# Performance work log

Hardware: AMD Instinct MI355X
Metric: run time of the kernel (lower is better)

The kernel has to match this reference:

```python
import jax, jax.numpy as jnp
import numpy as np

N = 4096          # number of leaves
M = 2 * N - 1     # total tree nodes
B = 256           # batch of distribution pairs


def setup_inputs() -> dict:
    key = jax.random.key(0)
    k0, k1, k2, k3, k4, k5 = jax.random.split(key, 6)
    # ancestor-indicator matrix: mostly zeros (structured sparse used densely)
    subtree = (jax.random.uniform(k0, (M, N)) < 0.01).astype(jnp.float32)
    d1 = jax.random.uniform(k1, (N, B), dtype=jnp.float32)
    d2 = jax.random.uniform(k2, (N, B), dtype=jnp.float32)
    ot_distances = jax.random.uniform(k3, (B,), dtype=jnp.float32)
    param = jax.random.normal(k4, (M,), dtype=jnp.float32)
    parents = jax.random.randint(k5, (M,), 0, M, dtype=jnp.int32)
    return {"d1": d1, "d2": d2, "ot_distances": ot_distances,
            "subtree": subtree, "param": param, "parents": parents}


def reference(d1, d2, ot_distances, subtree, param, parents):
    # aggregate leaf mass to every tree node: [M, B]
    m_d1 = jnp.matmul(subtree, d1)
    m_d2 = jnp.matmul(subtree, d2)
    # edge weight = parent height - node height: [M]
    w_v = param[parents] - param
    # tree-Wasserstein-1 per pair: [B]
    w1_tree = 0.5 * jnp.matmul(w_v, jnp.abs(m_d1 - m_d2))
    return jnp.sum(jnp.square(ot_distances - w1_tree))
```

## Files before the change

### kernel.cpp

```cpp
#include <hip/hip_runtime.h>
#include <hip/hip_fp8.h>

#define NN    4096
#define MM    8191
#define BB    256
#define CAP   256

typedef float nfloat4 __attribute__((ext_vector_type(4)));
typedef float f32x2 __attribute__((ext_vector_type(2)));

__device__ __forceinline__ int prefix_lt(unsigned long long m) {
    return __builtin_amdgcn_mbcnt_hi((unsigned)(m >> 32),
           __builtin_amdgcn_mbcnt_lo((unsigned)m, 0u));
}

#if defined(__has_builtin)
#if __has_builtin(__builtin_amdgcn_cvt_pk_fp8_f32) && __has_builtin(__builtin_amdgcn_cvt_pk_f32_fp8)
#define HW_FP8 1
#endif
#endif

__device__ __forceinline__ unsigned pack4fp8(float x0, float x1, float x2, float x3) {
#ifdef HW_FP8
    int r = 0;
    r = __builtin_amdgcn_cvt_pk_fp8_f32(x0, x1, r, false);
    r = __builtin_amdgcn_cvt_pk_fp8_f32(x2, x3, r, true);
    return (unsigned)r;
#else
    __hip_fp8_e4m3 a(x0), b(x1), c(x2), d(x3);
    return (unsigned)a.__x | ((unsigned)b.__x << 8) |
           ((unsigned)c.__x << 16) | ((unsigned)d.__x << 24);
#endif
}

__global__ __launch_bounds__(256) void k_prep(const float4* __restrict__ d1,
                                              const float4* __restrict__ d2,
                                              float* __restrict__ part2,
                                              unsigned* __restrict__ dd8) {
    int idx = blockIdx.x * 256 + threadIdx.x;
    if (idx < 256 * BB) part2[idx] = 0.0f;
    float4 a = d1[idx], b = d2[idx];
    dd8[idx] = pack4fp8(a.x - b.x, a.y - b.y, a.z - b.z, a.w - b.w);
}

__global__ __launch_bounds__(256, 4) void k_fused(
        const nfloat4* __restrict__ st4,
        const unsigned* __restrict__ dd8,
        const float* __restrict__ param,
        const int*   __restrict__ parents,
        float* __restrict__ part2) {
    __shared__ unsigned short s_idx[4][CAP];
    __shared__ float s_part[BB];
    const int tid  = threadIdx.x;
    const int wave = tid >> 6;
    const int lane = tid & 63;
    unsigned short* buf = s_idx[wave];

    s_part[tid] = 0.0f;
    __syncthreads();

    const int m = blockIdx.x * 4 + wave;
    if (m < MM) {
        int c = 0;
        #pragma unroll
        for (int h = 0; h < 2; ++h) {
            const nfloat4* base = st4 + (size_t)m * (NN / 4) + h * (NN / 8);
            nfloat4 v0 = __builtin_nontemporal_load(base + lane);
            nfloat4 v1 = __builtin_nontemporal_load(base + 64  + lane);
            nfloat4 v2 = __builtin_nontemporal_load(base + 128 + lane);
            nfloat4 v3 = __builtin_nontemporal_load(base + 192 + lane);
            nfloat4 v4 = __builtin_nontemporal_load(base + 256 + lane);
            nfloat4 v5 = __builtin_nontemporal_load(base + 320 + lane);
            nfloat4 v6 = __builtin_nontemporal_load(base + 384 + lane);
            nfloat4 v7 = __builtin_nontemporal_load(base + 448 + lane);

            const int cb = h * (NN / 2);
            #define SITE(val, col)                                          \
            {                                                               \
                unsigned long long mk = __ballot((val) != 0.0f);            \
                if ((val) != 0.0f)                                          \
                    buf[c + prefix_lt(mk)] = (unsigned short)(col);         \
                c += __popcll(mk);                                          \
            }
            #define QUAD(v, cb0)                                            \
                SITE(v.x, (cb0))     SITE(v.y, (cb0) + 1)                   \
                SITE(v.z, (cb0) + 2) SITE(v.w, (cb0) + 3)
            QUAD(v0, cb + (lane)       * 4)
            QUAD(v1, cb + (64  + lane) * 4)
            QUAD(v2, cb + (128 + lane) * 4)
            QUAD(v3, cb + (192 + lane) * 4)
            QUAD(v4, cb + (256 + lane) * 4)
            QUAD(v5, cb + (320 + lane) * 4)
            QUAD(v6, cb + (384 + lane) * 4)
            QUAD(v7, cb + (448 + lane) * 4)
            #undef QUAD
            #undef SITE
        }
        __builtin_amdgcn_wave_barrier();

        float c0 = 0.f, c1 = 0.f, c2 = 0.f, c3 = 0.f;
        float e0 = 0.f, e1 = 0.f, e2 = 0.f, e3 = 0.f;
#ifdef HW_FP8
        #define DEC(u, j0, j1, j2, j3)                                       \
        {                                                                    \
            f32x2 lo = __builtin_amdgcn_cvt_pk_f32_fp8((int)(u), false);     \
            f32x2 hi = __builtin_amdgcn_cvt_pk_f32_fp8((int)(u), true);      \
            j0 += lo.x; j1 += lo.y; j2 += hi.x; j3 += hi.y;                  \
        }
#else
        #define DEC(u, j0, j1, j2, j3)                                       \
        {                                                                    \
            __hip_fp8_e4m3 q0, q1, q2, q3;                                   \
            q0.__x = (unsigned char)(u);                                     \
            q1.__x = (unsigned char)((u) >> 8);                              \
            q2.__x = (unsigned char)((u) >> 16);                             \
            q3.__x = (unsigned char)((u) >> 24);                             \
            j0 += (float)q0; j1 += (float)q1; j2 += (float)q2; j3 += (float)q3; \
        }
#endif
        #define ACCA(u) DEC(u, c0, c1, c2, c3)
        #define ACCB(u) DEC(u, e0, e1, e2, e3)
        const unsigned* lw = (const unsigned*)buf;
        int i = 0;
        for (; i + 8 <= c; i += 8) {
            unsigned q0 = lw[(i >> 1)    ];
            unsigned q1 = lw[(i >> 1) + 1];
            unsigned q2 = lw[(i >> 1) + 2];
            unsigned q3 = lw[(i >> 1) + 3];
            unsigned g0 = dd8[(q0 & 0xffffu) * 64u + lane];
            unsigned g1 = dd8[(q0 >> 16)     * 64u + lane];
            unsigned g2 = dd8[(q1 & 0xffffu) * 64u + lane];
            unsigned g3 = dd8[(q1 >> 16)     * 64u + lane];
            unsigned g4 = dd8[(q2 & 0xffffu) * 64u + lane];
            unsigned g5 = dd8[(q2 >> 16)     * 64u + lane];
            unsigned g6 = dd8[(q3 & 0xffffu) * 64u + lane];
            unsigned g7 = dd8[(q3 >> 16)     * 64u + lane];
            ACCA(g0) ACCB(g1) ACCA(g2) ACCB(g3)
            ACCA(g4) ACCB(g5) ACCA(g6) ACCB(g7)
        }
        for (; i + 4 <= c; i += 4) {
            unsigned q0 = lw[(i >> 1)    ];
            unsigned q1 = lw[(i >> 1) + 1];
            unsigned g0 = dd8[(q0 & 0xffffu) * 64u + lane];
            unsigned g1 = dd8[(q0 >> 16)     * 64u + lane];
            unsigned g2 = dd8[(q1 & 0xffffu) * 64u + lane];
            unsigned g3 = dd8[(q1 >> 16)     * 64u + lane];
            ACCA(g0) ACCB(g1) ACCA(g2) ACCB(g3)
        }
        for (; i < c; ++i) {
            unsigned g = dd8[(unsigned)buf[i] * 64u + lane];
            ACCA(g)
        }
        #undef ACCA
        #undef ACCB
        #undef DEC

        const float wgt = param[parents[m]] - param[m];
        atomicAdd(&s_part[4 * lane + 0], wgt * fabsf(c0 + e0));
        atomicAdd(&s_part[4 * lane + 1], wgt * fabsf(c1 + e1));
        atomicAdd(&s_part[4 * lane + 2], wgt * fabsf(c2 + e2));
        atomicAdd(&s_part[4 * lane + 3], wgt * fabsf(c3 + e3));
    }
    __syncthreads();
    atomicAdd(&part2[(size_t)(blockIdx.x & 255) * BB + tid], s_part[tid]);
}

__global__ __launch_bounds__(1024) void k_finalize(const float* __restrict__ part2,
                                                   const float* __restrict__ ot,
                                                   float* __restrict__ out) {
    __shared__ float s_red[4][BB];
    __shared__ float s_sq[16];
    const int tid = threadIdx.x;
    const int s = tid >> 8, b = tid & 255;

    float a0 = 0.f, a1 = 0.f, a2 = 0.f, a3 = 0.f;
    float a4 = 0.f, a5 = 0.f, a6 = 0.f, a7 = 0.f;
    #pragma unroll
    for (int j = 0; j < 64; j += 8) {
        int row = s * 64 + j;
        a0 += part2[(row    ) * BB + b];
        a1 += part2[(row + 1) * BB + b];
        a2 += part2[(row + 2) * BB + b];
        a3 += part2[(row + 3) * BB + b];
        a4 += part2[(row + 4) * BB + b];
        a5 += part2[(row + 5) * BB + b];
        a6 += part2[(row + 6) * BB + b];
        a7 += part2[(row + 7) * BB + b];
    }
    s_red[s][b] = ((a0 + a1) + (a2 + a3)) + ((a4 + a5) + (a6 + a7));
    __syncthreads();

    float v = 0.0f;
    if (s == 0) {
        float w1 = (s_red[0][b] + s_red[1][b]) + (s_red[2][b] + s_red[3][b]);
        float e = ot[b] - 0.5f * w1;
        v = e * e;
    }
    #pragma unroll
    for (int off = 32; off > 0; off >>= 1) v += __shfl_down(v, off, 64);
    if ((tid & 63) == 0) s_sq[tid >> 6] = v;
    __syncthreads();
    if (tid == 0) out[0] = (s_sq[0] + s_sq[1]) + (s_sq[2] + s_sq[3]);
}

extern "C" void kernel_launch(void* const* d_in, const int* in_sizes, int n_in,
                              void* d_out, int out_size, void* d_ws, size_t ws_size,
                              hipStream_t stream) {
    const float* d1      = (const float*)d_in[0];
    const float* d2      = (const float*)d_in[1];
    const float* ot      = (const float*)d_in[2];
    const float* subtree = (const float*)d_in[3];
    const float* param   = (const float*)d_in[4];
    const int*   parents = (const int*)d_in[5];

    char* wsb = (char*)d_ws;
    float* part2   = (float*)wsb;
    unsigned* dd8  = (unsigned*)(wsb + 256 * BB * 4);

    k_prep<<<1024, 256, 0, stream>>>((const float4*)d1, (const float4*)d2,
                                     part2, dd8);
    k_fused<<<2048, 256, 0, stream>>>((const nfloat4*)subtree, dd8,
                                      param, parents, part2);
    k_finalize<<<1, 1024, 0, stream>>>(part2, ot, (float*)d_out);
}
```

Before: 47.25 us.

## Replicate packed fp8 difference table per XCD to localize gathers

The prep kernel now writes eight copies of the fp8-packed d1-d2 table when the workspace is large enough. Each block of the fused kernel reads the copy selected by its block index modulo eight, matching round-robin placement of blocks across dies. The aim is to keep each die's random gathers in its own L2 rather than sharing lines across dies. In exchange, the prep kernel does eight times the writes and re-reads of the inputs, and uses more workspace.

```diff
diff --git a/kernel.cpp b/kernel.cpp
--- a/kernel.cpp
+++ b/kernel.cpp
@@ -36,11 +36,16 @@
 __global__ __launch_bounds__(256) void k_prep(const float4* __restrict__ d1,
                                               const float4* __restrict__ d2,
                                               float* __restrict__ part2,
-                                              unsigned* __restrict__ dd8) {
-    int idx = blockIdx.x * 256 + threadIdx.x;
-    if (idx < 256 * BB) part2[idx] = 0.0f;
+                                              unsigned* __restrict__ dd8,
+                                              int repmask) {
+    const int p   = blockIdx.x;
+    const int r   = p & repmask;
+    const int s   = p >> (repmask ? 3 : 0);
+    const int idx = s * 256 + (int)threadIdx.x;
+    if (r == 0 && idx < 256 * BB) part2[idx] = 0.0f;
     float4 a = d1[idx], b = d2[idx];
-    dd8[idx] = pack4fp8(a.x - b.x, a.y - b.y, a.z - b.z, a.w - b.w);
+    dd8[(size_t)r * (NN * BB / 4) + idx] =
+        pack4fp8(a.x - b.x, a.y - b.y, a.z - b.z, a.w - b.w);
 }
 
 __global__ __launch_bounds__(256, 4) void k_fused(
@@ -48,13 +53,15 @@
         const unsigned* __restrict__ dd8,
         const float* __restrict__ param,
         const int*   __restrict__ parents,
-        float* __restrict__ part2) {
+        float* __restrict__ part2,
+        int repmask) {
     __shared__ unsigned short s_idx[4][CAP];
     __shared__ float s_part[BB];
     const int tid  = threadIdx.x;
     const int wave = tid >> 6;
     const int lane = tid & 63;
     unsigned short* buf = s_idx[wave];
+    const unsigned* ddl = dd8 + (size_t)(blockIdx.x & repmask) * (NN * BB / 4);
 
     s_part[tid] = 0.0f;
     __syncthreads();
@@ -127,28 +134,28 @@
             unsigned q1 = lw[(i >> 1) + 1];
             unsigned q2 = lw[(i >> 1) + 2];
             unsigned q3 = lw[(i >> 1) + 3];
-            unsigned g0 = dd8[(q0 & 0xffffu) * 64u + lane];
-            unsigned g1 = dd8[(q0 >> 16)     * 64u + lane];
-            unsigned g2 = dd8[(q1 & 0xffffu) * 64u + lane];
-            unsigned g3 = dd8[(q1 >> 16)     * 64u + lane];
-            unsigned g4 = dd8[(q2 & 0xffffu) * 64u + lane];
-            unsigned g5 = dd8[(q2 >> 16)     * 64u + lane];
-            unsigned g6 = dd8[(q3 & 0xffffu) * 64u + lane];
-            unsigned g7 = dd8[(q3 >> 16)     * 64u + lane];
+            unsigned g0 = ddl[(q0 & 0xffffu) * 64u + lane];
+            unsigned g1 = ddl[(q0 >> 16)     * 64u + lane];
+            unsigned g2 = ddl[(q1 & 0xffffu) * 64u + lane];
+            unsigned g3 = ddl[(q1 >> 16)     * 64u + lane];
+            unsigned g4 = ddl[(q2 & 0xffffu) * 64u + lane];
+            unsigned g5 = ddl[(q2 >> 16)     * 64u + lane];
+            unsigned g6 = ddl[(q3 & 0xffffu) * 64u + lane];
+            unsigned g7 = ddl[(q3 >> 16)     * 64u + lane];
             ACCA(g0) ACCB(g1) ACCA(g2) ACCB(g3)
             ACCA(g4) ACCB(g5) ACCA(g6) ACCB(g7)
         }
         for (; i + 4 <= c; i += 4) {
             unsigned q0 = lw[(i >> 1)    ];
             unsigned q1 = lw[(i >> 1) + 1];
-            unsigned g0 = dd8[(q0 & 0xffffu) * 64u + lane];
-            unsigned g1 = dd8[(q0 >> 16)     * 64u + lane];
-            unsigned g2 = dd8[(q1 & 0xffffu) * 64u + lane];
-            unsigned g3 = dd8[(q1 >> 16)     * 64u + lane];
+            unsigned g0 = ddl[(q0 & 0xffffu) * 64u + lane];
+            unsigned g1 = ddl[(q0 >> 16)     * 64u + lane];
+            unsigned g2 = ddl[(q1 & 0xffffu) * 64u + lane];
+            unsigned g3 = ddl[(q1 >> 16)     * 64u + lane];
             ACCA(g0) ACCB(g1) ACCA(g2) ACCB(g3)
         }
         for (; i < c; ++i) {
-            unsigned g = dd8[(unsigned)buf[i] * 64u + lane];
+            unsigned g = ddl[(unsigned)buf[i] * 64u + lane];
             ACCA(g)
         }
         #undef ACCA
@@ -214,12 +221,16 @@
     const int*   parents = (const int*)d_in[5];
 
     char* wsb = (char*)d_ws;
-    float* part2   = (float*)wsb;
-    unsigned* dd8  = (unsigned*)(wsb + 256 * BB * 4);
-
-    k_prep<<<1024, 256, 0, stream>>>((const float4*)d1, (const float4*)d2,
-                                     part2, dd8);
+    float* part2  = (float*)wsb;
+    unsigned* dd8 = (unsigned*)(wsb + 256 * BB * 4);
+
+    const size_t need8 = 256 * BB * 4 + (size_t)8 * NN * BB;
+    const int nrep = (ws_size >= need8) ? 8 : 1;
+    const int repmask = nrep - 1;
+
+    k_prep<<<1024 * nrep, 256, 0, stream>>>((const float4*)d1, (const float4*)d2,
+                                            part2, dd8, repmask);
     k_fused<<<2048, 256, 0, stream>>>((const nfloat4*)subtree, dd8,
-                                      param, parents, part2);
+                                      param, parents, part2, repmask);
     k_finalize<<<1, 1024, 0, stream>>>(part2, ot, (float*)d_out);
 }
```

Result: slower. 56.47 us (+19.5%).

## Split compaction from gather and stage batch slabs of dd8 in shared memory

Applied to the files above, without the earlier changes.

The fused kernel is split in two. A compaction kernel writes per-row nonzero column lists to global memory. A slab kernel then loads a 16-column batch slab of the FP8 difference matrix (64 KB) into LDS and gathers from LDS instead of from global/L2. Blocks are tiled over 16 batch slabs and 32 row groups, and partial sums are written directly instead of with global atomics. The cost is an extra launch, a global round trip for the index lists, and 64 KB of LDS per block, which limits occupancy.

```diff
diff --git a/kernel.cpp b/kernel.cpp
--- a/kernel.cpp
+++ b/kernel.cpp
@@ -5,6 +5,9 @@
 #define MM    8191
 #define BB    256
 #define CAP   256
+#define NSLAB 16
+#define SLABW 16
+#define NPART 512
 
 typedef float nfloat4 __attribute__((ext_vector_type(4)));
 typedef float f32x2 __attribute__((ext_vector_type(2)));
@@ -33,136 +36,155 @@
 #endif
 }
 
+__device__ __forceinline__ void dec4fp8(unsigned g, float& x0, float& x1,
+                                        float& x2, float& x3) {
+#ifdef HW_FP8
+    f32x2 lo = __builtin_amdgcn_cvt_pk_f32_fp8((int)g, false);
+    f32x2 hi = __builtin_amdgcn_cvt_pk_f32_fp8((int)g, true);
+    x0 = lo.x; x1 = lo.y; x2 = hi.x; x3 = hi.y;
+#else
+    __hip_fp8_e4m3 q0, q1, q2, q3;
+    q0.__x = (unsigned char)g;
+    q1.__x = (unsigned char)(g >> 8);
+    q2.__x = (unsigned char)(g >> 16);
+    q3.__x = (unsigned char)(g >> 24);
+    x0 = (float)q0; x1 = (float)q1; x2 = (float)q2; x3 = (float)q3;
+#endif
+}
+
 __global__ __launch_bounds__(256) void k_prep(const float4* __restrict__ d1,
                                               const float4* __restrict__ d2,
                                               float* __restrict__ part2,
                                               unsigned* __restrict__ dd8) {
     int idx = blockIdx.x * 256 + threadIdx.x;
-    if (idx < 256 * BB) part2[idx] = 0.0f;
+    if (idx < NPART * BB) part2[idx] = 0.0f;
     float4 a = d1[idx], b = d2[idx];
     dd8[idx] = pack4fp8(a.x - b.x, a.y - b.y, a.z - b.z, a.w - b.w);
 }
 
-__global__ __launch_bounds__(256, 4) void k_fused(
+__global__ __launch_bounds__(256, 4) void k_compact(
         const nfloat4* __restrict__ st4,
+        int* __restrict__ cnt,
+        unsigned short* __restrict__ list) {
+    __shared__ unsigned short s_buf[4][CAP];
+    const int wave = threadIdx.x >> 6;
+    const int lane = threadIdx.x & 63;
+    unsigned short* buf = s_buf[wave];
+    const int m = blockIdx.x * 4 + wave;
+    if (m >= MM) return;
+
+    int c = 0;
+    #pragma unroll
+    for (int h = 0; h < 2; ++h) {
+        const nfloat4* base = st4 + (size_t)m * (NN / 4) + h * (NN / 8);
+        nfloat4 v0 = __builtin_nontemporal_load(base + lane);
+        nfloat4 v1 = __builtin_nontemporal_load(base + 64  + lane);
+        nfloat4 v2 = __builtin_nontemporal_load(base + 128 + lane);
+        nfloat4 v3 = __builtin_nontemporal_load(base + 192 + lane);
+        nfloat4 v4 = __builtin_nontemporal_load(base + 256 + lane);
+        nfloat4 v5 = __builtin_nontemporal_load(base + 320 + lane);
+        nfloat4 v6 = __builtin_nontemporal_load(base + 384 + lane);
+        nfloat4 v7 = __builtin_nontemporal_load(base + 448 + lane);
+
+        const int cb = h * (NN / 2);
+        #define SITE(val, col)                                          \
+        {                                                               \
+            unsigned long long mk = __ballot((val) != 0.0f);            \
+            if ((val) != 0.0f)                                          \
+                buf[c + prefix_lt(mk)] = (unsigned short)(col);         \
+            c += __popcll(mk);                                          \
+        }
+        #define QUAD(v, cb0)                                            \
+            SITE(v.x, (cb0))     SITE(v.y, (cb0) + 1)                   \
+            SITE(v.z, (cb0) + 2) SITE(v.w, (cb0) + 3)
+        QUAD(v0, cb + (lane)       * 4)
+        QUAD(v1, cb + (64  + lane) * 4)
+        QUAD(v2, cb + (128 + lane) * 4)
+        QUAD(v3, cb + (192 + lane) * 4)
+        QUAD(v4, cb + (256 + lane) * 4)
+        QUAD(v5, cb + (320 + lane) * 4)
+        QUAD(v6, cb + (384 + lane) * 4)
+        QUAD(v7, cb + (448 + lane) * 4)
+        #undef QUAD
+        #undef SITE
+    }
+    __builtin_amdgcn_wave_barrier();
+
+    if (lane == 0) cnt[m] = c;
+    uint4* lv = (uint4*)(list + (size_t)m * CAP);
+    const int nv = (c + 7) >> 3;
+    if (lane < nv) lv[lane] = ((const uint4*)s_buf[wave])[lane];
+}
+
+__global__ __launch_bounds__(512, 4) void k_slab(
         const unsigned* __restrict__ dd8,
+        const int* __restrict__ cnt,
+        const unsigned short* __restrict__ list,
         const float* __restrict__ param,
         const int*   __restrict__ parents,
         float* __restrict__ part2) {
-    __shared__ unsigned short s_idx[4][CAP];
-    __shared__ float s_part[BB];
+    __shared__ unsigned s_dd[NN * 4];
+    __shared__ float s_part[SLABW];
     const int tid  = threadIdx.x;
     const int wave = tid >> 6;
     const int lane = tid & 63;
-    unsigned short* buf = s_idx[wave];
-
-    s_part[tid] = 0.0f;
-    __syncthreads();
-
-    const int m = blockIdx.x * 4 + wave;
-    if (m < MM) {
-        int c = 0;
+    const int s    = blockIdx.x & (NSLAB - 1);
+    const int rg   = blockIdx.x >> 4;
+
+    if (tid < SLABW) s_part[tid] = 0.0f;
+    #pragma unroll
+    for (int i = 0; i < 32; ++i) {
+        int t = tid + i * 512;
+        int n = t >> 2, j = t & 3;
+        s_dd[t] = dd8[(size_t)n * 64 + s * 4 + j];
+    }
+    __syncthreads();
+
+    const int j   = lane & 3;
+    const int sub = lane >> 2;
+    float p0 = 0.f, p1 = 0.f, p2 = 0.f, p3 = 0.f;
+
+    for (int r = 0; r < 32; ++r) {
+        const int m = rg * 256 + wave * 32 + r;
+        if (m >= MM) break;
+        int c = cnt[m];
+        if (c > CAP) c = CAP;
+        const unsigned short* lp = list + (size_t)m * CAP;
+
+        float a0 = 0.f, a1 = 0.f, a2 = 0.f, a3 = 0.f;
+        for (int it = 0; it * 16 < c; ++it) {
+            int i = it * 16 + sub;
+            if (i < c) {
+                unsigned n = lp[i];
+                unsigned g = s_dd[n * 4 + j];
+                float x0, x1, x2, x3;
+                dec4fp8(g, x0, x1, x2, x3);
+                a0 += x0; a1 += x1; a2 += x2; a3 += x3;
+            }
+        }
         #pragma unroll
-        for (int h = 0; h < 2; ++h) {
-            const nfloat4* base = st4 + (size_t)m * (NN / 4) + h * (NN / 8);
-            nfloat4 v0 = __builtin_nontemporal_load(base + lane);
-            nfloat4 v1 = __builtin_nontemporal_load(base + 64  + lane);
-            nfloat4 v2 = __builtin_nontemporal_load(base + 128 + lane);
-            nfloat4 v3 = __builtin_nontemporal_load(base + 192 + lane);
-            nfloat4 v4 = __builtin_nontemporal_load(base + 256 + lane);
-            nfloat4 v5 = __builtin_nontemporal_load(base + 320 + lane);
-            nfloat4 v6 = __builtin_nontemporal_load(base + 384 + lane);
-            nfloat4 v7 = __builtin_nontemporal_load(base + 448 + lane);
-
-            const int cb = h * (NN / 2);
-            #define SITE(val, col)                                          \
-            {                                                               \
-                unsigned long long mk = __ballot((val) != 0.0f);            \
-                if ((val) != 0.0f)                                          \
-                    buf[c + prefix_lt(mk)] = (unsigned short)(col);         \
-                c += __popcll(mk);                                          \
-            }
-            #define QUAD(v, cb0)                                            \
-                SITE(v.x, (cb0))     SITE(v.y, (cb0) + 1)                   \
-                SITE(v.z, (cb0) + 2) SITE(v.w, (cb0) + 3)
-            QUAD(v0, cb + (lane)       * 4)
-            QUAD(v1, cb + (64  + lane) * 4)
-            QUAD(v2, cb + (128 + lane) * 4)
-            QUAD(v3, cb + (192 + lane) * 4)
-            QUAD(v4, cb + (256 + lane) * 4)
-            QUAD(v5, cb + (320 + lane) * 4)
-            QUAD(v6, cb + (384 + lane) * 4)
-            QUAD(v7, cb + (448 + lane) * 4)
-            #undef QUAD
-            #undef SITE
+        for (int off = 4; off <= 32; off <<= 1) {
+            a0 += __shfl_xor(a0, off, 64);
+            a1 += __shfl_xor(a1, off, 64);
+            a2 += __shfl_xor(a2, off, 64);
+            a3 += __shfl_xor(a3, off, 64);
         }
-        __builtin_amdgcn_wave_barrier();
-
-        float c0 = 0.f, c1 = 0.f, c2 = 0.f, c3 = 0.f;
-        float e0 = 0.f, e1 = 0.f, e2 = 0.f, e3 = 0.f;
-#ifdef HW_FP8
-        #define DEC(u, j0, j1, j2, j3)                                       \
-        {                                                                    \
-            f32x2 lo = __builtin_amdgcn_cvt_pk_f32_fp8((int)(u), false);     \
-            f32x2 hi = __builtin_amdgcn_cvt_pk_f32_fp8((int)(u), true);      \
-            j0 += lo.x; j1 += lo.y; j2 += hi.x; j3 += hi.y;                  \
-        }
-#else
-        #define DEC(u, j0, j1, j2, j3)                                       \
-        {                                                                    \
-            __hip_fp8_e4m3 q0, q1, q2, q3;                                   \
-            q0.__x = (unsigned char)(u);                                     \
-            q1.__x = (unsigned char)((u) >> 8);                              \
-            q2.__x = (unsigned char)((u) >> 16);                             \
-            q3.__x = (unsigned char)((u) >> 24);                             \
-            j0 += (float)q0; j1 += (float)q1; j2 += (float)q2; j3 += (float)q3; \
-        }
-#endif
-        #define ACCA(u) DEC(u, c0, c1, c2, c3)
-        #define ACCB(u) DEC(u, e0, e1, e2, e3)
-        const unsigned* lw = (const unsigned*)buf;
-        int i = 0;
-        for (; i + 8 <= c; i += 8) {
-            unsigned q0 = lw[(i >> 1)    ];
-            unsigned q1 = lw[(i >> 1) + 1];
-            unsigned q2 = lw[(i >> 1) + 2];
-            unsigned q3 = lw[(i >> 1) + 3];
-            unsigned g0 = dd8[(q0 & 0xffffu) * 64u + lane];
-            unsigned g1 = dd8[(q0 >> 16)     * 64u + lane];
-            unsigned g2 = dd8[(q1 & 0xffffu) * 64u + lane];
-            unsigned g3 = dd8[(q1 >> 16)     * 64u + lane];
-            unsigned g4 = dd8[(q2 & 0xffffu) * 64u + lane];
-            unsigned g5 = dd8[(q2 >> 16)     * 64u + lane];
-            unsigned g6 = dd8[(q3 & 0xffffu) * 64u + lane];
-            unsigned g7 = dd8[(q3 >> 16)     * 64u + lane];
-            ACCA(g0) ACCB(g1) ACCA(g2) ACCB(g3)
-            ACCA(g4) ACCB(g5) ACCA(g6) ACCB(g7)
-        }
-        for (; i + 4 <= c; i += 4) {
-            unsigned q0 = lw[(i >> 1)    ];
-            unsigned q1 = lw[(i >> 1) + 1];
-            unsigned g0 = dd8[(q0 & 0xffffu) * 64u + lane];
-            unsigned g1 = dd8[(q0 >> 16)     * 64u + lane];
-            unsigned g2 = dd8[(q1 & 0xffffu) * 64u + lane];
-            unsigned g3 = dd8[(q1 >> 16)     * 64u + lane];
-            ACCA(g0) ACCB(g1) ACCA(g2) ACCB(g3)
-        }
-        for (; i < c; ++i) {
-            unsigned g = dd8[(unsigned)buf[i] * 64u + lane];
-            ACCA(g)
-        }
-        #undef ACCA
-        #undef ACCB
-        #undef DEC
-
         const float wgt = param[parents[m]] - param[m];
-        atomicAdd(&s_part[4 * lane + 0], wgt * fabsf(c0 + e0));
-        atomicAdd(&s_part[4 * lane + 1], wgt * fabsf(c1 + e1));
-        atomicAdd(&s_part[4 * lane + 2], wgt * fabsf(c2 + e2));
-        atomicAdd(&s_part[4 * lane + 3], wgt * fabsf(c3 + e3));
-    }
-    __syncthreads();
-    atomicAdd(&part2[(size_t)(blockIdx.x & 255) * BB + tid], s_part[tid]);
+        p0 += wgt * fabsf(a0);
+        p1 += wgt * fabsf(a1);
+        p2 += wgt * fabsf(a2);
+        p3 += wgt * fabsf(a3);
+    }
+
+    if (lane < 4) {
+        atomicAdd(&s_part[lane * 4 + 0], p0);
+        atomicAdd(&s_part[lane * 4 + 1], p1);
+        atomicAdd(&s_part[lane * 4 + 2], p2);
+        atomicAdd(&s_part[lane * 4 + 3], p3);
+    }
+    __syncthreads();
+    if (tid < SLABW)
+        part2[(size_t)blockIdx.x * BB + s * SLABW + tid] = s_part[tid];
 }
 
 __global__ __launch_bounds__(1024) void k_finalize(const float* __restrict__ part2,
@@ -171,13 +193,13 @@
     __shared__ float s_red[4][BB];
     __shared__ float s_sq[16];
     const int tid = threadIdx.x;
-    const int s = tid >> 8, b = tid & 255;
+    const int sl = tid >> 8, b = tid & 255;
 
     float a0 = 0.f, a1 = 0.f, a2 = 0.f, a3 = 0.f;
     float a4 = 0.f, a5 = 0.f, a6 = 0.f, a7 = 0.f;
     #pragma unroll
-    for (int j = 0; j < 64; j += 8) {
-        int row = s * 64 + j;
+    for (int jj = 0; jj < 128; jj += 8) {
+        int row = sl * 128 + jj;
         a0 += part2[(row    ) * BB + b];
         a1 += part2[(row + 1) * BB + b];
         a2 += part2[(row + 2) * BB + b];
@@ -187,11 +209,11 @@
         a6 += part2[(row + 6) * BB + b];
         a7 += part2[(row + 7) * BB + b];
     }
-    s_red[s][b] = ((a0 + a1) + (a2 + a3)) + ((a4 + a5) + (a6 + a7));
+    s_red[sl][b] = ((a0 + a1) + (a2 + a3)) + ((a4 + a5) + (a6 + a7));
     __syncthreads();
 
     float v = 0.0f;
-    if (s == 0) {
+    if (sl == 0) {
         float w1 = (s_red[0][b] + s_red[1][b]) + (s_red[2][b] + s_red[3][b]);
         float e = ot[b] - 0.5f * w1;
         v = e * e;
@@ -214,12 +236,17 @@
     const int*   parents = (const int*)d_in[5];
 
     char* wsb = (char*)d_ws;
-    float* part2   = (float*)wsb;
-    unsigned* dd8  = (unsigned*)(wsb + 256 * BB * 4);
+    float* part2 = (float*)wsb;
+    size_t off = (size_t)NPART * BB * 4;
+    unsigned* dd8 = (unsigned*)(wsb + off);
+    off += (size_t)NN * BB;
+    int* cnt = (int*)(wsb + off);
+    off += ((size_t)MM * 4 + 15) & ~(size_t)15;
+    unsigned short* list = (unsigned short*)(wsb + off);
 
     k_prep<<<1024, 256, 0, stream>>>((const float4*)d1, (const float4*)d2,
                                      part2, dd8);
-    k_fused<<<2048, 256, 0, stream>>>((const nfloat4*)subtree, dd8,
-                                      param, parents, part2);
+    k_compact<<<2048, 256, 0, stream>>>((const nfloat4*)subtree, cnt, list);
+    k_slab<<<NPART, 512, 0, stream>>>(dd8, cnt, list, param, parents, part2);
     k_finalize<<<1, 1024, 0, stream>>>(part2, ot, (float*)d_out);
 }
```

New measurement: 101.7 us. +115.3%, slower.
